# Kernel tuning notes

Measured on AMD Instinct MI355X. Metric: run time of the kernel, lower is better.

## Reference

```python
import jax, jax.numpy as jnp
import numpy as np

N = 8192
E = 524288
IN_DIM = 128
HID = 256
OUT_DIM = 128
N_LAYERS = 3
N_HEADS = 4
HEAD_DIM = HID // N_HEADS


def setup_inputs() -> dict:
    key = jax.random.key(0)
    ks = jax.random.split(key, 12)
    s = 0.05
    return {
        "x": jax.random.normal(ks[0], (N, IN_DIM), dtype=jnp.float32),
        "edge_index": jax.random.randint(ks[1], (2, E), 0, N, dtype=jnp.int64),
        "W_in": jax.random.normal(ks[2], (HID, IN_DIM), dtype=jnp.float32) * s,
        "b_in": jnp.zeros((HID,), dtype=jnp.float32),
        "plasticity": jnp.ones((N_LAYERS,), dtype=jnp.float32),
        "synaptic": jnp.ones((N_LAYERS,), dtype=jnp.float32),
        "in_proj_w": jax.random.normal(ks[3], (3 * HID, HID), dtype=jnp.float32) * s,
        "in_proj_b": jnp.zeros((3 * HID,), dtype=jnp.float32),
        "out_proj_w": jax.random.normal(ks[4], (HID, HID), dtype=jnp.float32) * s,
        "out_proj_b": jnp.zeros((HID,), dtype=jnp.float32),
        "W_out": jax.random.normal(ks[5], (OUT_DIM, HID), dtype=jnp.float32) * s,
        "b_out": jnp.zeros((OUT_DIM,), dtype=jnp.float32),
    }


def _forward(x, edge_index, W_in, b_in, plasticity, synaptic,
             in_proj_w, in_proj_b, out_proj_w, out_proj_b, W_out, b_out):
    src, dst = edge_index[0], edge_index[1]  # x_j = x[src], aggregate at dst (source_to_target)
    x = x @ W_in.T + b_in  # [N, HID]
    for i in range(N_LAYERS):
        x = x * jax.nn.sigmoid(plasticity[i])
        # message: x_j * sigmoid(synaptic) (scalar edge weight); aggr='add'
        agg = jax.ops.segment_sum(x[src], dst, num_segments=N)  # gather-scatter-add
        x = jax.nn.leaky_relu(agg * jax.nn.sigmoid(synaptic[i]), negative_slope=0.01)
    # MultiheadAttention over all N nodes (seq_len=N, batch=1)
    qkv = x @ in_proj_w.T + in_proj_b  # [N, 3*HID]
    q, k, v = jnp.split(qkv, 3, axis=-1)
    q = q.reshape(N, N_HEADS, HEAD_DIM).transpose(1, 0, 2)  # [h, n, d]
    k = k.reshape(N, N_HEADS, HEAD_DIM).transpose(1, 0, 2)
    v = v.reshape(N, N_HEADS, HEAD_DIM).transpose(1, 0, 2)
    scores = jnp.einsum("hnd,hmd->hnm", q, k) / np.sqrt(HEAD_DIM).astype(np.float32)
    attn = jax.nn.softmax(scores, axis=-1)
    o = jnp.einsum("hnm,hmd->hnd", attn, v)  # [h, n, d]
    o = o.transpose(1, 0, 2).reshape(N, HID)
    x = o @ out_proj_w.T + out_proj_b
    return x @ W_out.T + b_out  # [N, OUT_DIM]


def reference(x, edge_index, W_in, b_in, plasticity, synaptic,
              in_proj_w, in_proj_b, out_proj_w, out_proj_b, W_out, b_out):
    return _forward(x, edge_index, W_in, b_in, plasticity, synaptic,
                    in_proj_w, in_proj_b, out_proj_w, out_proj_b, W_out, b_out)
```

## Files before the change

### kernel.cpp

```cpp
#include <hip/hip_runtime.h>
#include <hip/hip_bf16.h>
#include <float.h>

#define N_NODES 8192
#define NEDGE   524288
#define IND     128
#define HID     256
#define OUTD    128
#define NHEAD   4
#define HD      64

typedef short short8 __attribute__((ext_vector_type(8)));
typedef float f32x4  __attribute__((ext_vector_type(4)));
typedef float f32x16 __attribute__((ext_vector_type(16)));
typedef unsigned int u32x4 __attribute__((ext_vector_type(4)));

__device__ __forceinline__ float sigmoidf_(float x) { return 1.0f / (1.0f + expf(-x)); }

__device__ __forceinline__ unsigned short f2bf(float f) {
    __hip_bfloat16 b = __float2bfloat16(f);
    return __builtin_bit_cast(unsigned short, b);
}
__device__ __forceinline__ float bf2f(unsigned short u) {
    __hip_bfloat16 b = __builtin_bit_cast(__hip_bfloat16, u);
    return __bfloat162float(b);
}
__device__ __forceinline__ void split3(float x, unsigned short& a, unsigned short& b, unsigned short& c) {
    a = f2bf(x); float r = x - bf2f(a);
    b = f2bf(r); r = r - bf2f(b);
    c = f2bf(r);
}
__device__ __forceinline__ unsigned int cvtpk(float lo, float hi) {
    unsigned int r;
    asm("v_cvt_pk_bf16_f32 %0, %1, %2" : "=v"(r) : "v"(lo), "v"(hi));
    return r;
}
__device__ __forceinline__ void plswap(unsigned int& a, unsigned int& b) {
    asm volatile("v_permlane32_swap_b32 %0, %1" : "+v"(a), "+v"(b));
}

__device__ __forceinline__ void gll16(const void* g, void* l) {
    __builtin_amdgcn_global_load_lds(
        (const __attribute__((address_space(1))) void*)g,
        (__attribute__((address_space(3))) void*)l, 16, 0, 0);
}

__device__ __forceinline__ f32x16 mfma32(short8 a, short8 b, f32x16 c) {
    return __builtin_amdgcn_mfma_f32_32x32x16_bf16(a, b, c, 0, 0, 0);
}

__global__ __launch_bounds__(256) void gemm_bias_kernel(
    const float* __restrict__ A, const float* __restrict__ W,
    const float* __restrict__ bias, float* __restrict__ C,
    int M, int Nn, int K)
{
    __shared__ float As[64][33];
    __shared__ float Ws[64][33];
    const int t  = threadIdx.x;
    const int tx = t & 15, ty = t >> 4;
    const int m0 = blockIdx.x * 64, n0 = blockIdx.y * 64;
    const int lr = t >> 2;
    const int lc = (t & 3) * 8;

    float acc[4][4] = {};
    for (int kk = 0; kk < K; kk += 32) {
        const float* Ap = A + (size_t)(m0 + lr) * K + kk + lc;
        const float* Wp = W + (size_t)(n0 + lr) * K + kk + lc;
        float4 a0 = *(const float4*)(Ap);
        float4 a1 = *(const float4*)(Ap + 4);
        float4 w0 = *(const float4*)(Wp);
        float4 w1 = *(const float4*)(Wp + 4);
        __syncthreads();
        As[lr][lc + 0] = a0.x; As[lr][lc + 1] = a0.y; As[lr][lc + 2] = a0.z; As[lr][lc + 3] = a0.w;
        As[lr][lc + 4] = a1.x; As[lr][lc + 5] = a1.y; As[lr][lc + 6] = a1.z; As[lr][lc + 7] = a1.w;
        Ws[lr][lc + 0] = w0.x; Ws[lr][lc + 1] = w0.y; Ws[lr][lc + 2] = w0.z; Ws[lr][lc + 3] = w0.w;
        Ws[lr][lc + 4] = w1.x; Ws[lr][lc + 5] = w1.y; Ws[lr][lc + 6] = w1.z; Ws[lr][lc + 7] = w1.w;
        __syncthreads();
        #pragma unroll 8
        for (int k = 0; k < 32; ++k) {
            float a[4], w[4];
            #pragma unroll
            for (int i = 0; i < 4; ++i) a[i] = As[ty * 4 + i][k];
            #pragma unroll
            for (int j = 0; j < 4; ++j) w[j] = Ws[tx * 4 + j][k];
            #pragma unroll
            for (int i = 0; i < 4; ++i)
                #pragma unroll
                for (int j = 0; j < 4; ++j)
                    acc[i][j] += a[i] * w[j];
        }
    }
    #pragma unroll
    for (int i = 0; i < 4; ++i) {
        const int m = m0 + ty * 4 + i;
        #pragma unroll
        for (int j = 0; j < 4; ++j) {
            const int n = n0 + tx * 4 + j;
            C[(size_t)m * Nn + n] = acc[i][j] + bias[n];
        }
    }
}

__global__ void hist_kernel(const int* __restrict__ ei, int* __restrict__ deg)
{
    int e = blockIdx.x * blockDim.x + threadIdx.x;
    if (e < NEDGE) atomicAdd(&deg[ei[NEDGE + e]], 1);
}

__global__ __launch_bounds__(1024) void scan_kernel(
    const int* __restrict__ deg, int* __restrict__ row_ptr, int* __restrict__ cursor)
{
    __shared__ int sh[1024];
    const int t = threadIdx.x;
    int v[8]; int s = 0;
    #pragma unroll
    for (int i = 0; i < 8; ++i) { v[i] = deg[t * 8 + i]; s += v[i]; }
    sh[t] = s; __syncthreads();
    for (int off = 1; off < 1024; off <<= 1) {
        int add = (t >= off) ? sh[t - off] : 0;
        __syncthreads();
        sh[t] += add;
        __syncthreads();
    }
    int base = sh[t] - s;
    #pragma unroll
    for (int i = 0; i < 8; ++i) {
        row_ptr[t * 8 + i] = base;
        cursor[t * 8 + i]  = base;
        base += v[i];
    }
    if (t == 1023) row_ptr[N_NODES] = base;
}

__global__ void scatter_kernel(const int* __restrict__ ei, int* __restrict__ cursor,
                               int* __restrict__ esrc)
{
    int e = blockIdx.x * blockDim.x + threadIdx.x;
    if (e < NEDGE) {
        int d = ei[NEDGE + e];
        int p = atomicAdd(&cursor[d], 1);
        esrc[p] = ei[e];
    }
}

__global__ __launch_bounds__(256) void aggregate_kernel(
    const float* __restrict__ hin, float* __restrict__ hout,
    const int* __restrict__ row_ptr, const int* __restrict__ esrc,
    const float* __restrict__ plas, const float* __restrict__ syn, int layer)
{
    const int b = blockIdx.x;
    const int c = threadIdx.x;
    const int st = row_ptr[b], en = row_ptr[b + 1];
    float a0 = 0.f, a1 = 0.f, a2 = 0.f, a3 = 0.f;
    int e = st;
    for (; e + 4 <= en; e += 4) {
        int s0 = esrc[e], s1 = esrc[e + 1], s2 = esrc[e + 2], s3 = esrc[e + 3];
        a0 += hin[(size_t)s0 * HID + c];
        a1 += hin[(size_t)s1 * HID + c];
        a2 += hin[(size_t)s2 * HID + c];
        a3 += hin[(size_t)s3 * HID + c];
    }
    float acc = (a0 + a1) + (a2 + a3);
    for (; e < en; ++e) acc += hin[(size_t)esrc[e] * HID + c];
    const float scale = sigmoidf_(plas[layer]) * sigmoidf_(syn[layer]);
    float x = acc * scale;
    hout[(size_t)b * HID + c] = (x > 0.f) ? x : 0.01f * x;
}

__global__ __launch_bounds__(256) void split_kernel(
    const float* __restrict__ qkv,
    unsigned short* __restrict__ Kc0, unsigned short* __restrict__ Kc1,
    unsigned short* __restrict__ Kc2, unsigned short* __restrict__ Vt0)
{
    __shared__ unsigned short vts[64 * 80];
    const int h  = blockIdx.y;
    const int n0 = blockIdx.x * 64;
    const int t  = threadIdx.x;
    const int r  = t >> 2;
    const int n  = n0 + r;
    const int dc = (t & 3) * 16;

    {
        const float* kp = qkv + (size_t)n * 768 + 256 + h * 64 + dc;
        float kv[16];
        #pragma unroll
        for (int i = 0; i < 16; i += 4) {
            float4 f = *(const float4*)(kp + i);
            kv[i] = f.x; kv[i+1] = f.y; kv[i+2] = f.z; kv[i+3] = f.w;
        }
        #pragma unroll
        for (int half = 0; half < 2; ++half) {
            short8 c0, c1, c2;
            #pragma unroll
            for (int j = 0; j < 8; ++j) {
                unsigned short a, b, c;
                split3(kv[half * 8 + j], a, b, c);
                c0[j] = (short)a; c1[j] = (short)b; c2[j] = (short)c;
            }
            const int pos = ((dc >> 3) + half) ^ ((n >> 2) & 7);
            const size_t base = ((size_t)(h * 8192 + n)) * 64 + pos * 8;
            *(short8*)(Kc0 + base) = c0;
            *(short8*)(Kc1 + base) = c1;
            *(short8*)(Kc2 + base) = c2;
        }
    }
    {
        const float* vp = qkv + (size_t)n * 768 + 512 + h * 64 + dc;
        #pragma unroll
        for (int i = 0; i < 16; i += 4) {
            float4 f = *(const float4*)(vp + i);
            float vv[4] = {f.x, f.y, f.z, f.w};
            #pragma unroll
            for (int k2 = 0; k2 < 4; ++k2)
                vts[(dc + i + k2) * 80 + r] = f2bf(vv[k2]);
        }
    }
    __syncthreads();
    #pragma unroll
    for (int i = 0; i < 2; ++i) {
        const int q = t * 2 + i;
        const int d = q >> 3, nc = q & 7;
        short8 vv = *(const short8*)(&vts[d * 80 + nc * 8]);
        const size_t dst = ((size_t)(h * 64 + d)) * 8192 + n0 + ((nc ^ ((d >> 2) & 7)) * 8);
        *(short8*)(Vt0 + dst) = vv;
    }
}

__global__ __launch_bounds__(256, 1) void attn_mfma_kernel(
    const float* __restrict__ qkv,
    const unsigned short* __restrict__ Kc0, const unsigned short* __restrict__ Kc1,
    const unsigned short* __restrict__ Kc2, const unsigned short* __restrict__ Vt0,
    float* __restrict__ Op, float* __restrict__ Ml)
{
    __shared__ __align__(16) char smem[65536];
    const int h    = blockIdx.y;
    const int half = blockIdx.z;
    const int n0   = blockIdx.x * 256;
    const int t    = threadIdx.x;
    const int wv   = t >> 6;
    const int lane = t & 63;
    const int l31  = lane & 31, l5 = lane >> 5;
    const int qbase = n0 + wv * 64;

    short8 qf[2][3][4];
    #pragma unroll
    for (int qb = 0; qb < 2; ++qb) {
        #pragma unroll
        for (int ks = 0; ks < 4; ++ks) {
            const float* qp = qkv + (size_t)(qbase + qb * 32 + l31) * 768 + h * 64 + ks * 16 + l5 * 8;
            float4 qa = *(const float4*)qp, qb4 = *(const float4*)(qp + 4);
            float qv[8] = {qa.x, qa.y, qa.z, qa.w, qb4.x, qb4.y, qb4.z, qb4.w};
            #pragma unroll
            for (int j = 0; j < 8; ++j) {
                unsigned short a, b, c;
                split3(qv[j] * 0.125f, a, b, c);
                qf[qb][0][ks][j] = (short)a;
                qf[qb][1][ks][j] = (short)b;
                qf[qb][2][ks][j] = (short)c;
            }
        }
    }

    const unsigned short* cbase = (wv == 0) ? Kc0 : (wv == 1) ? Kc1 : (wv == 2) ? Kc2 : Vt0;
    const char* sgb[8];
    #pragma unroll
    for (int s = 0; s < 8; ++s) {
        const int row = s * 8 + (lane >> 3);
        if (wv < 3)
            sgb[s] = (const char*)(cbase + ((size_t)(h * 8192 + row)) * 64 + (lane & 7) * 8);
        else
            sgb[s] = (const char*)(cbase + ((size_t)(h * 64 + row)) * 8192 + (lane & 7) * 8);
    }
    const size_t ktstride = (wv < 3) ? 8192 : 128;
    const int ldsbase = wv * 8192;

    auto STAGE = [&](int ktg, int bb) {
        #pragma unroll
        for (int s = 0; s < 8; ++s)
            gll16(sgb[s] + (size_t)ktg * ktstride, &smem[bb * 32768 + ldsbase + s * 1024]);
    };

    f32x16 o[2][2];
    #pragma unroll
    for (int db = 0; db < 2; ++db)
        #pragma unroll
        for (int qb = 0; qb < 2; ++qb)
            #pragma unroll
            for (int r = 0; r < 16; ++r) o[db][qb][r] = 0.f;
    float mr[2] = {-FLT_MAX, -FLT_MAX};
    float ls[2] = {0.f, 0.f};

    const int kt0 = half * 64;
    STAGE(kt0, 0);
    __syncthreads();

    for (int kt = 0; kt < 64; ++kt) {
        const int bb = kt & 1;
        if (kt < 63) STAGE(kt0 + kt + 1, bb ^ 1);
        const char* buf = &smem[bb * 32768];

        f32x16 s[2][2];
        #pragma unroll
        for (int kb = 0; kb < 2; ++kb)
            #pragma unroll
            for (int qb = 0; qb < 2; ++qb)
                #pragma unroll
                for (int r = 0; r < 16; ++r) s[kb][qb][r] = 0.f;

        #pragma unroll
        for (int ks = 0; ks < 4; ++ks) {
            #pragma unroll
            for (int kb = 0; kb < 2; ++kb) {
                const int key = kb * 32 + l31;
                const int off = key * 128 + (((ks * 2 + l5) ^ ((key >> 2) & 7)) * 16);
                short8 k0 = *(const short8*)(buf + off);
                short8 k1 = *(const short8*)(buf + 8192 + off);
                short8 k2 = *(const short8*)(buf + 16384 + off);
                #pragma unroll
                for (int qb = 0; qb < 2; ++qb) {
                    f32x16 acc = s[kb][qb];
                    acc = mfma32(k0, qf[qb][2][ks], acc);
                    acc = mfma32(k1, qf[qb][1][ks], acc);
                    acc = mfma32(k2, qf[qb][0][ks], acc);
                    acc = mfma32(k0, qf[qb][1][ks], acc);
                    acc = mfma32(k1, qf[qb][0][ks], acc);
                    acc = mfma32(k0, qf[qb][0][ks], acc);
                    s[kb][qb] = acc;
                }
            }
        }

        short8 pb[2][4];
        #pragma unroll
        for (int qb = 0; qb < 2; ++qb) {
            float mx = s[0][qb][0];
            #pragma unroll
            for (int r = 1; r < 16; ++r) mx = fmaxf(mx, s[0][qb][r]);
            #pragma unroll
            for (int r = 0; r < 16; ++r) mx = fmaxf(mx, s[1][qb][r]);
            mx = fmaxf(mx, __shfl_xor(mx, 32));
            const float mn = fmaxf(mr[qb], mx);
            const float alpha = __expf(mr[qb] - mn);
            mr[qb] = mn;
            float ps = 0.f;
            #pragma unroll
            for (int kb = 0; kb < 2; ++kb)
                #pragma unroll
                for (int r = 0; r < 16; ++r) {
                    float p = __expf(s[kb][qb][r] - mn);
                    s[kb][qb][r] = p;
                    ps += p;
                }
            ps += __shfl_xor(ps, 32);
            ls[qb] = ls[qb] * alpha + ps;
            o[0][qb] *= alpha;
            o[1][qb] *= alpha;

            #pragma unroll
            for (int ks = 0; ks < 4; ++ks) {
                const int kb = ks >> 1, rb = (ks & 1) * 8;
                unsigned int A0 = cvtpk(s[kb][qb][rb + 0], s[kb][qb][rb + 1]);
                unsigned int A1 = cvtpk(s[kb][qb][rb + 2], s[kb][qb][rb + 3]);
                unsigned int B0 = cvtpk(s[kb][qb][rb + 4], s[kb][qb][rb + 5]);
                unsigned int B1 = cvtpk(s[kb][qb][rb + 6], s[kb][qb][rb + 7]);
                plswap(A0, B0);
                plswap(A1, B1);
                u32x4 pw; pw[0] = A0; pw[1] = A1; pw[2] = B0; pw[3] = B1;
                pb[qb][ks] = __builtin_bit_cast(short8, pw);
            }
        }

        #pragma unroll
        for (int ks = 0; ks < 4; ++ks) {
            #pragma unroll
            for (int db = 0; db < 2; ++db) {
                const int d = db * 32 + l31;
                const int off = 24576 + d * 128 + (((ks * 2 + l5) ^ ((d >> 2) & 7)) * 16);
                short8 v = *(const short8*)(buf + off);
                o[db][0] = mfma32(v, pb[0][ks], o[db][0]);
                o[db][1] = mfma32(v, pb[1][ks], o[db][1]);
            }
        }

        __syncthreads();
    }

    #pragma unroll
    for (int qb = 0; qb < 2; ++qb) {
        const int q = qbase + qb * 32 + l31;
        float* opq = Op + ((size_t)((half * 4 + h) * 8192 + q)) * 64;
        #pragma unroll
        for (int db = 0; db < 2; ++db) {
            #pragma unroll
            for (int tq = 0; tq < 4; ++tq) {
                float4 st = { o[db][qb][4 * tq + 0], o[db][qb][4 * tq + 1],
                              o[db][qb][4 * tq + 2], o[db][qb][4 * tq + 3] };
                *(float4*)(opq + db * 32 + tq * 8 + l5 * 4) = st;
            }
        }
        if (l5 == 0) {
            Ml[((size_t)(half * 4 + h) * 2 + 0) * 8192 + q] = mr[qb];
            Ml[((size_t)(half * 4 + h) * 2 + 1) * 8192 + q] = ls[qb];
        }
    }
}

__global__ __launch_bounds__(256) void combine_kernel(
    const float* __restrict__ Op, const float* __restrict__ Ml, float* __restrict__ aO)
{
    const int idx = blockIdx.x * 256 + threadIdx.x;
    const int c = idx & 3;
    const int q = (idx >> 2) & 8191;
    const int h = idx >> 15;
    const float m0 = Ml[((size_t)(0 + h) * 2 + 0) * 8192 + q];
    const float l0 = Ml[((size_t)(0 + h) * 2 + 1) * 8192 + q];
    const float m1 = Ml[((size_t)(4 + h) * 2 + 0) * 8192 + q];
    const float l1 = Ml[((size_t)(4 + h) * 2 + 1) * 8192 + q];
    const float m  = fmaxf(m0, m1);
    const float c0 = __expf(m0 - m), c1 = __expf(m1 - m);
    const float inv = 1.f / (l0 * c0 + l1 * c1);
    const float* p0 = Op + ((size_t)(0 + h) * 8192 + q) * 64 + c * 16;
    const float* p1 = Op + ((size_t)(4 + h) * 8192 + q) * 64 + c * 16;
    float* dst = aO + (size_t)q * 256 + h * 64 + c * 16;
    #pragma unroll
    for (int i = 0; i < 4; ++i) {
        float4 a = *(const float4*)(p0 + i * 4);
        float4 b = *(const float4*)(p1 + i * 4);
        float4 r = { (a.x * c0 + b.x * c1) * inv, (a.y * c0 + b.y * c1) * inv,
                     (a.z * c0 + b.z * c1) * inv, (a.w * c0 + b.w * c1) * inv };
        *(float4*)(dst + i * 4) = r;
    }
}

extern "C" void kernel_launch(void* const* d_in, const int* in_sizes, int n_in,
                              void* d_out, int out_size, void* d_ws, size_t ws_size,
                              hipStream_t stream)
{
    const float* x     = (const float*)d_in[0];
    const int*   ei    = (const int*)  d_in[1];
    const float* W_in  = (const float*)d_in[2];
    const float* b_in  = (const float*)d_in[3];
    const float* plas  = (const float*)d_in[4];
    const float* syn   = (const float*)d_in[5];
    const float* inpw  = (const float*)d_in[6];
    const float* inpb  = (const float*)d_in[7];
    const float* outpw = (const float*)d_in[8];
    const float* outpb = (const float*)d_in[9];
    const float* Wout  = (const float*)d_in[10];
    const float* bout  = (const float*)d_in[11];
    float* out = (float*)d_out;

    char* ws = (char*)d_ws;
    float* h    = (float*)(ws + 0);
    float* h2   = (float*)(ws + (8u  << 20));
    float* qkv  = (float*)(ws + (16u << 20));
    float* Op   = (float*)(ws + (40u << 20));
    float* aO   = (float*)(ws + 0);
    float* tmp  = (float*)(ws + (48u << 20));
    unsigned short* Kc0 = (unsigned short*)(ws + 0);
    unsigned short* Kc1 = (unsigned short*)(ws + (4u  << 20));
    unsigned short* Kc2 = (unsigned short*)(ws + (8u  << 20));
    unsigned short* Vt0 = (unsigned short*)(ws + (12u << 20));
    int*   rowp = (int*)(ws + (56u << 20));
    int*   curs = (int*)(ws + (56u << 20) + 40960);
    int*   esrc = (int*)(ws + (56u << 20) + 81920);
    float* Ml   = (float*)(ws + (56u << 20) + 81920);

    hipMemsetAsync(curs, 0, N_NODES * sizeof(int), stream);
    hist_kernel<<<NEDGE / 256, 256, 0, stream>>>(ei, curs);
    scan_kernel<<<1, 1024, 0, stream>>>(curs, rowp, curs);
    scatter_kernel<<<NEDGE / 256, 256, 0, stream>>>(ei, curs, esrc);

    gemm_bias_kernel<<<dim3(N_NODES / 64, HID / 64), 256, 0, stream>>>(
        x, W_in, b_in, h, N_NODES, HID, IND);

    aggregate_kernel<<<N_NODES, 256, 0, stream>>>(h,  h2, rowp, esrc, plas, syn, 0);
    aggregate_kernel<<<N_NODES, 256, 0, stream>>>(h2, h,  rowp, esrc, plas, syn, 1);
    aggregate_kernel<<<N_NODES, 256, 0, stream>>>(h,  h2, rowp, esrc, plas, syn, 2);

    gemm_bias_kernel<<<dim3(N_NODES / 64, 768 / 64), 256, 0, stream>>>(
        h2, inpw, inpb, qkv, N_NODES, 768, HID);

    split_kernel<<<dim3(N_NODES / 64, NHEAD), 256, 0, stream>>>(
        qkv, Kc0, Kc1, Kc2, Vt0);

    attn_mfma_kernel<<<dim3(N_NODES / 256, NHEAD, 2), 256, 0, stream>>>(
        qkv, Kc0, Kc1, Kc2, Vt0, Op, Ml);

    combine_kernel<<<512, 256, 0, stream>>>(Op, Ml, aO);

    gemm_bias_kernel<<<dim3(N_NODES / 64, HID / 64), 256, 0, stream>>>(
        aO, outpw, outpb, tmp, N_NODES, HID, HID);
    gemm_bias_kernel<<<dim3(N_NODES / 64, OUTD / 64), 256, 0, stream>>>(
        tmp, Wout, bout, out, N_NODES, OUTD, HID);
}
```

Before: 610.7 us.

## Split attention keys four ways, bf16 partials, lazy rescale, larger GEMM tiles

The attention kernel now splits the key range into four chunks instead of two and allows two blocks per CU. It adds s_setprio around the MFMA phases and skips the online-softmax rescale unless the running max grows by more than 8. Partial outputs are stored as bf16, and the combine kernel merges four partials. The LDS swizzle for K/V changes to XOR with the low row bits, and the fp32 GEMM uses 128x64 tiles with vectorized LDS stores. The aim is more parallelism and latency hiding in attention and less partial-output traffic, at the cost of bf16 rounding in the partials and more combine work.

```diff
diff --git a/kernel.cpp b/kernel.cpp
--- a/kernel.cpp
+++ b/kernel.cpp
@@ -38,13 +38,11 @@
 __device__ __forceinline__ void plswap(unsigned int& a, unsigned int& b) {
     asm volatile("v_permlane32_swap_b32 %0, %1" : "+v"(a), "+v"(b));
 }
-
 __device__ __forceinline__ void gll16(const void* g, void* l) {
     __builtin_amdgcn_global_load_lds(
         (const __attribute__((address_space(1))) void*)g,
         (__attribute__((address_space(3))) void*)l, 16, 0, 0);
 }
-
 __device__ __forceinline__ f32x16 mfma32(short8 a, short8 b, f32x16 c) {
     return __builtin_amdgcn_mfma_f32_32x32x16_bf16(a, b, c, 0, 0, 0);
 }
@@ -54,45 +52,49 @@
     const float* __restrict__ bias, float* __restrict__ C,
     int M, int Nn, int K)
 {
-    __shared__ float As[64][33];
+    __shared__ float As[128][33];
     __shared__ float Ws[64][33];
     const int t  = threadIdx.x;
     const int tx = t & 15, ty = t >> 4;
-    const int m0 = blockIdx.x * 64, n0 = blockIdx.y * 64;
-    const int lr = t >> 2;
-    const int lc = (t & 3) * 8;
-
-    float acc[4][4] = {};
+    const int m0 = blockIdx.x * 128, n0 = blockIdx.y * 64;
+    const int alr = t >> 1, alc = (t & 1) * 16;
+    const int wlr = t >> 2, wlc = (t & 3) * 8;
+
+    float acc[8][4] = {};
     for (int kk = 0; kk < K; kk += 32) {
-        const float* Ap = A + (size_t)(m0 + lr) * K + kk + lc;
-        const float* Wp = W + (size_t)(n0 + lr) * K + kk + lc;
+        const float* Ap = A + (size_t)(m0 + alr) * K + kk + alc;
+        const float* Wp = W + (size_t)(n0 + wlr) * K + kk + wlc;
         float4 a0 = *(const float4*)(Ap);
         float4 a1 = *(const float4*)(Ap + 4);
+        float4 a2 = *(const float4*)(Ap + 8);
+        float4 a3 = *(const float4*)(Ap + 12);
         float4 w0 = *(const float4*)(Wp);
         float4 w1 = *(const float4*)(Wp + 4);
         __syncthreads();
-        As[lr][lc + 0] = a0.x; As[lr][lc + 1] = a0.y; As[lr][lc + 2] = a0.z; As[lr][lc + 3] = a0.w;
-        As[lr][lc + 4] = a1.x; As[lr][lc + 5] = a1.y; As[lr][lc + 6] = a1.z; As[lr][lc + 7] = a1.w;
-        Ws[lr][lc + 0] = w0.x; Ws[lr][lc + 1] = w0.y; Ws[lr][lc + 2] = w0.z; Ws[lr][lc + 3] = w0.w;
-        Ws[lr][lc + 4] = w1.x; Ws[lr][lc + 5] = w1.y; Ws[lr][lc + 6] = w1.z; Ws[lr][lc + 7] = w1.w;
+        *(float4*)(&As[alr][alc + 0])  = a0;
+        *(float4*)(&As[alr][alc + 4])  = a1;
+        *(float4*)(&As[alr][alc + 8])  = a2;
+        *(float4*)(&As[alr][alc + 12]) = a3;
+        *(float4*)(&Ws[wlr][wlc + 0])  = w0;
+        *(float4*)(&Ws[wlr][wlc + 4])  = w1;
         __syncthreads();
-        #pragma unroll 8
+        #pragma unroll 4
         for (int k = 0; k < 32; ++k) {
-            float a[4], w[4];
-            #pragma unroll
-            for (int i = 0; i < 4; ++i) a[i] = As[ty * 4 + i][k];
+            float a[8], w[4];
+            #pragma unroll
+            for (int i = 0; i < 8; ++i) a[i] = As[ty * 8 + i][k];
             #pragma unroll
             for (int j = 0; j < 4; ++j) w[j] = Ws[tx * 4 + j][k];
             #pragma unroll
-            for (int i = 0; i < 4; ++i)
+            for (int i = 0; i < 8; ++i)
                 #pragma unroll
                 for (int j = 0; j < 4; ++j)
                     acc[i][j] += a[i] * w[j];
         }
     }
     #pragma unroll
-    for (int i = 0; i < 4; ++i) {
-        const int m = m0 + ty * 4 + i;
+    for (int i = 0; i < 8; ++i) {
+        const int m = m0 + ty * 8 + i;
         #pragma unroll
         for (int j = 0; j < 4; ++j) {
             const int n = n0 + tx * 4 + j;
@@ -197,7 +199,7 @@
                 split3(kv[half * 8 + j], a, b, c);
                 c0[j] = (short)a; c1[j] = (short)b; c2[j] = (short)c;
             }
-            const int pos = ((dc >> 3) + half) ^ ((n >> 2) & 7);
+            const int pos = ((dc >> 3) + half) ^ (n & 7);
             const size_t base = ((size_t)(h * 8192 + n)) * 64 + pos * 8;
             *(short8*)(Kc0 + base) = c0;
             *(short8*)(Kc1 + base) = c1;
@@ -221,20 +223,20 @@
         const int q = t * 2 + i;
         const int d = q >> 3, nc = q & 7;
         short8 vv = *(const short8*)(&vts[d * 80 + nc * 8]);
-        const size_t dst = ((size_t)(h * 64 + d)) * 8192 + n0 + ((nc ^ ((d >> 2) & 7)) * 8);
+        const size_t dst = ((size_t)(h * 64 + d)) * 8192 + n0 + ((nc ^ (d & 7)) * 8);
         *(short8*)(Vt0 + dst) = vv;
     }
 }
 
-__global__ __launch_bounds__(256, 1) void attn_mfma_kernel(
+__global__ __launch_bounds__(256, 2) void attn_mfma_kernel(
     const float* __restrict__ qkv,
     const unsigned short* __restrict__ Kc0, const unsigned short* __restrict__ Kc1,
     const unsigned short* __restrict__ Kc2, const unsigned short* __restrict__ Vt0,
-    float* __restrict__ Op, float* __restrict__ Ml)
+    unsigned short* __restrict__ Op16, float* __restrict__ Ml)
 {
     __shared__ __align__(16) char smem[65536];
     const int h    = blockIdx.y;
-    const int half = blockIdx.z;
+    const int quar = blockIdx.z;
     const int n0   = blockIdx.x * 256;
     const int t    = threadIdx.x;
     const int wv   = t >> 6;
@@ -290,13 +292,13 @@
     float mr[2] = {-FLT_MAX, -FLT_MAX};
     float ls[2] = {0.f, 0.f};
 
-    const int kt0 = half * 64;
+    const int kt0 = quar * 32;
     STAGE(kt0, 0);
     __syncthreads();
 
-    for (int kt = 0; kt < 64; ++kt) {
+    for (int kt = 0; kt < 32; ++kt) {
         const int bb = kt & 1;
-        if (kt < 63) STAGE(kt0 + kt + 1, bb ^ 1);
+        if (kt < 31) STAGE(kt0 + kt + 1, bb ^ 1);
         const char* buf = &smem[bb * 32768];
 
         f32x16 s[2][2];
@@ -307,12 +309,13 @@
                 #pragma unroll
                 for (int r = 0; r < 16; ++r) s[kb][qb][r] = 0.f;
 
+        __builtin_amdgcn_s_setprio(1);
         #pragma unroll
         for (int ks = 0; ks < 4; ++ks) {
             #pragma unroll
             for (int kb = 0; kb < 2; ++kb) {
                 const int key = kb * 32 + l31;
-                const int off = key * 128 + (((ks * 2 + l5) ^ ((key >> 2) & 7)) * 16);
+                const int off = key * 128 + (((ks * 2 + l5) ^ (key & 7)) * 16);
                 short8 k0 = *(const short8*)(buf + off);
                 short8 k1 = *(const short8*)(buf + 8192 + off);
                 short8 k2 = *(const short8*)(buf + 16384 + off);
@@ -329,6 +332,7 @@
                 }
             }
         }
+        __builtin_amdgcn_s_setprio(0);
 
         short8 pb[2][4];
         #pragma unroll
@@ -339,22 +343,26 @@
             #pragma unroll
             for (int r = 0; r < 16; ++r) mx = fmaxf(mx, s[1][qb][r]);
             mx = fmaxf(mx, __shfl_xor(mx, 32));
-            const float mn = fmaxf(mr[qb], mx);
-            const float alpha = __expf(mr[qb] - mn);
-            mr[qb] = mn;
+            if (__any(mx > mr[qb] + 8.f)) {
+                const float mn = fmaxf(mr[qb], mx);
+                const float alpha = __expf(mr[qb] - mn);
+                mr[qb] = mn;
+                ls[qb] *= alpha;
+                o[0][qb] *= alpha;
+                o[1][qb] *= alpha;
+            }
+            const float mkeep = mr[qb];
             float ps = 0.f;
             #pragma unroll
             for (int kb = 0; kb < 2; ++kb)
                 #pragma unroll
                 for (int r = 0; r < 16; ++r) {
-                    float p = __expf(s[kb][qb][r] - mn);
+                    float p = __expf(s[kb][qb][r] - mkeep);
                     s[kb][qb][r] = p;
                     ps += p;
                 }
             ps += __shfl_xor(ps, 32);
-            ls[qb] = ls[qb] * alpha + ps;
-            o[0][qb] *= alpha;
-            o[1][qb] *= alpha;
+            ls[qb] += ps;
 
             #pragma unroll
             for (int ks = 0; ks < 4; ++ks) {
@@ -370,17 +378,19 @@
             }
         }
 
+        __builtin_amdgcn_s_setprio(1);
         #pragma unroll
         for (int ks = 0; ks < 4; ++ks) {
             #pragma unroll
             for (int db = 0; db < 2; ++db) {
                 const int d = db * 32 + l31;
-                const int off = 24576 + d * 128 + (((ks * 2 + l5) ^ ((d >> 2) & 7)) * 16);
+                const int off = 24576 + d * 128 + (((ks * 2 + l5) ^ (d & 7)) * 16);
                 short8 v = *(const short8*)(buf + off);
                 o[db][0] = mfma32(v, pb[0][ks], o[db][0]);
                 o[db][1] = mfma32(v, pb[1][ks], o[db][1]);
             }
         }
+        __builtin_amdgcn_s_setprio(0);
 
         __syncthreads();
     }
@@ -388,46 +398,64 @@
     #pragma unroll
     for (int qb = 0; qb < 2; ++qb) {
         const int q = qbase + qb * 32 + l31;
-        float* opq = Op + ((size_t)((half * 4 + h) * 8192 + q)) * 64;
+        unsigned short* opq = Op16 + ((size_t)((quar * 4 + h) * 8192 + q)) * 64;
         #pragma unroll
         for (int db = 0; db < 2; ++db) {
             #pragma unroll
             for (int tq = 0; tq < 4; ++tq) {
-                float4 st = { o[db][qb][4 * tq + 0], o[db][qb][4 * tq + 1],
-                              o[db][qb][4 * tq + 2], o[db][qb][4 * tq + 3] };
-                *(float4*)(opq + db * 32 + tq * 8 + l5 * 4) = st;
+                const int d0 = db * 32 + tq * 8 + l5 * 4;
+                unsigned int w0 = cvtpk(o[db][qb][4 * tq + 0], o[db][qb][4 * tq + 1]);
+                unsigned int w1 = cvtpk(o[db][qb][4 * tq + 2], o[db][qb][4 * tq + 3]);
+                uint2 st = {w0, w1};
+                *(uint2*)(opq + d0) = st;
             }
         }
         if (l5 == 0) {
-            Ml[((size_t)(half * 4 + h) * 2 + 0) * 8192 + q] = mr[qb];
-            Ml[((size_t)(half * 4 + h) * 2 + 1) * 8192 + q] = ls[qb];
+            Ml[((size_t)(quar * 4 + h) * 2 + 0) * 8192 + q] = mr[qb];
+            Ml[((size_t)(quar * 4 + h) * 2 + 1) * 8192 + q] = ls[qb];
         }
     }
 }
 
 __global__ __launch_bounds__(256) void combine_kernel(
-    const float* __restrict__ Op, const float* __restrict__ Ml, float* __restrict__ aO)
+    const unsigned short* __restrict__ Op16, const float* __restrict__ Ml,
+    float* __restrict__ aO)
 {
     const int idx = blockIdx.x * 256 + threadIdx.x;
     const int c = idx & 3;
     const int q = (idx >> 2) & 8191;
     const int h = idx >> 15;
-    const float m0 = Ml[((size_t)(0 + h) * 2 + 0) * 8192 + q];
-    const float l0 = Ml[((size_t)(0 + h) * 2 + 1) * 8192 + q];
-    const float m1 = Ml[((size_t)(4 + h) * 2 + 0) * 8192 + q];
-    const float l1 = Ml[((size_t)(4 + h) * 2 + 1) * 8192 + q];
-    const float m  = fmaxf(m0, m1);
-    const float c0 = __expf(m0 - m), c1 = __expf(m1 - m);
-    const float inv = 1.f / (l0 * c0 + l1 * c1);
-    const float* p0 = Op + ((size_t)(0 + h) * 8192 + q) * 64 + c * 16;
-    const float* p1 = Op + ((size_t)(4 + h) * 8192 + q) * 64 + c * 16;
+    float m[4], l[4];
+    float mg = -FLT_MAX;
+    #pragma unroll
+    for (int s = 0; s < 4; ++s) {
+        m[s] = Ml[((size_t)(s * 4 + h) * 2 + 0) * 8192 + q];
+        l[s] = Ml[((size_t)(s * 4 + h) * 2 + 1) * 8192 + q];
+        mg = fmaxf(mg, m[s]);
+    }
+    float w[4], denom = 0.f;
+    #pragma unroll
+    for (int s = 0; s < 4; ++s) {
+        w[s] = __expf(m[s] - mg);
+        denom += l[s] * w[s];
+    }
+    const float inv = 1.f / denom;
+    float acc[16] = {};
+    #pragma unroll
+    for (int s = 0; s < 4; ++s) {
+        const unsigned short* p = Op16 + ((size_t)(s * 4 + h) * 8192 + q) * 64 + c * 16;
+        short8 v0 = *(const short8*)(p);
+        short8 v1 = *(const short8*)(p + 8);
+        #pragma unroll
+        for (int i = 0; i < 8; ++i) {
+            acc[i]     += w[s] * bf2f((unsigned short)v0[i]);
+            acc[i + 8] += w[s] * bf2f((unsigned short)v1[i]);
+        }
+    }
     float* dst = aO + (size_t)q * 256 + h * 64 + c * 16;
     #pragma unroll
     for (int i = 0; i < 4; ++i) {
-        float4 a = *(const float4*)(p0 + i * 4);
-        float4 b = *(const float4*)(p1 + i * 4);
-        float4 r = { (a.x * c0 + b.x * c1) * inv, (a.y * c0 + b.y * c1) * inv,
-                     (a.z * c0 + b.z * c1) * inv, (a.w * c0 + b.w * c1) * inv };
+        float4 r = { acc[4*i] * inv, acc[4*i+1] * inv, acc[4*i+2] * inv, acc[4*i+3] * inv };
         *(float4*)(dst + i * 4) = r;
     }
 }
@@ -454,9 +482,9 @@
     float* h    = (float*)(ws + 0);
     float* h2   = (float*)(ws + (8u  << 20));
     float* qkv  = (float*)(ws + (16u << 20));
-    float* Op   = (float*)(ws + (40u << 20));
     float* aO   = (float*)(ws + 0);
     float* tmp  = (float*)(ws + (48u << 20));
+    unsigned short* Op16 = (unsigned short*)(ws + (40u << 20));
     unsigned short* Kc0 = (unsigned short*)(ws + 0);
     unsigned short* Kc1 = (unsigned short*)(ws + (4u  << 20));
     unsigned short* Kc2 = (unsigned short*)(ws + (8u  << 20));
@@ -471,26 +499,26 @@
     scan_kernel<<<1, 1024, 0, stream>>>(curs, rowp, curs);
     scatter_kernel<<<NEDGE / 256, 256, 0, stream>>>(ei, curs, esrc);
 
-    gemm_bias_kernel<<<dim3(N_NODES / 64, HID / 64), 256, 0, stream>>>(
+    gemm_bias_kernel<<<dim3(N_NODES / 128, HID / 64), 256, 0, stream>>>(
         x, W_in, b_in, h, N_NODES, HID, IND);
 
     aggregate_kernel<<<N_NODES, 256, 0, stream>>>(h,  h2, rowp, esrc, plas, syn, 0);
     aggregate_kernel<<<N_NODES, 256, 0, stream>>>(h2, h,  rowp, esrc, plas, syn, 1);
     aggregate_kernel<<<N_NODES, 256, 0, stream>>>(h,  h2, rowp, esrc, plas, syn, 2);
 
-    gemm_bias_kernel<<<dim3(N_NODES / 64, 768 / 64), 256, 0, stream>>>(
+    gemm_bias_kernel<<<dim3(N_NODES / 128, 768 / 64), 256, 0, stream>>>(
         h2, inpw, inpb, qkv, N_NODES, 768, HID);
 
     split_kernel<<<dim3(N_NODES / 64, NHEAD), 256, 0, stream>>>(
         qkv, Kc0, Kc1, Kc2, Vt0);
 
-    attn_mfma_kernel<<<dim3(N_NODES / 256, NHEAD, 2), 256, 0, stream>>>(
-        qkv, Kc0, Kc1, Kc2, Vt0, Op, Ml);
-
-    combine_kernel<<<512, 256, 0, stream>>>(Op, Ml, aO);
-
-    gemm_bias_kernel<<<dim3(N_NODES / 64, HID / 64), 256, 0, stream>>>(
+    attn_mfma_kernel<<<dim3(N_NODES / 256, NHEAD, 4), 256, 0, stream>>>(
+        qkv, Kc0, Kc1, Kc2, Vt0, Op16, Ml);
+
+    combine_kernel<<<512, 256, 0, stream>>>(Op16, Ml, aO);
+
+    gemm_bias_kernel<<<dim3(N_NODES / 128, HID / 64), 256, 0, stream>>>(
         aO, outpw, outpb, tmp, N_NODES, HID, HID);
-    gemm_bias_kernel<<<dim3(N_NODES / 64, OUTD / 64), 256, 0, stream>>>(
+    gemm_bias_kernel<<<dim3(N_NODES / 128, OUTD / 64), 256, 0, stream>>>(
         tmp, Wout, bout, out, N_NODES, OUTD, HID);
 }
```

Measured after the change: 590.1 us. -3.4%, faster.
